# Optimization experiments

Measured on AMD Instinct MI355X. Metric: run time of the kernel, lower is better.

The kernel has to match this reference:

```python
import jax, jax.numpy as jnp
import numpy as np

EMBED_DIMS = 192
NUM_HEADS = 6
WH, WW = 7, 7
N_TOK = WH * WW
B_WIN = 4096


def _rpe_index(Wh, Ww):
    coords = np.array([[x, y] for x in range(Ww) for y in range(Wh)])  # [N,2]
    d = coords[None, :, :] - coords[:, None, :]                        # [N,N,2]
    idx = (d[:, :, 0] + Ww - 1) * (2 * Ww - 1) + (d[:, :, 1] + Wh - 1)
    return idx.T  # transpose(0,1) as in the torch code


def setup_inputs() -> dict:
    key = jax.random.key(0)
    ks = jax.random.split(key, 6)
    C = EMBED_DIMS
    return {
        "x": jax.random.normal(ks[0], (B_WIN, N_TOK, C), dtype=jnp.float32),
        "qkv_w": jax.random.normal(ks[1], (3 * C, C), dtype=jnp.float32) * 0.02,
        "qkv_b": jax.random.normal(ks[2], (3 * C,), dtype=jnp.float32) * 0.02,
        "proj_w": jax.random.normal(ks[3], (C, C), dtype=jnp.float32) * 0.02,
        "proj_b": jax.random.normal(ks[4], (C,), dtype=jnp.float32) * 0.02,
        "rpe_table": jax.random.normal(ks[5], ((2 * WH - 1) * (2 * WW - 1), NUM_HEADS), dtype=jnp.float32),
        "rpe_idx": jnp.asarray(_rpe_index(WH, WW), dtype=jnp.int32),
    }


def reference(x, qkv_w, qkv_b, proj_w, proj_b, rpe_table, rpe_idx):
    B, N, C = x.shape
    H = NUM_HEADS
    hd = C // H
    scale = hd ** -0.5
    # qkv projection: torch Linear is x @ W.T + b
    qkv = x @ qkv_w.T + qkv_b                      # [B, N, 3C]
    qkv = qkv.reshape(B, N, 3, H, hd).transpose(2, 0, 3, 1, 4)  # [3, B, H, N, hd]
    q, k, v = qkv[0] * scale, qkv[1], qkv[2]
    attn = jnp.einsum("bhnd,bhmd->bhnm", q, k)     # [B, H, N, N]
    # relative position bias gather: table[idx] -> [N, N, H] -> [H, N, N]
    bias = rpe_table[rpe_idx].transpose(2, 0, 1)
    attn = jax.nn.softmax(attn + bias, axis=-1)
    out = jnp.einsum("bhnm,bhmd->bhnd", attn, v)   # [B, H, N, hd]
    out = out.transpose(0, 2, 1, 3).reshape(B, N, C)
    return out @ proj_w.T + proj_b
```

## Files before the change

kernel.cpp:

```cpp
#include <hip/hip_runtime.h>
#include <stdint.h>

#define NWIN 4096
#define NTOK 49
#define CDIM 192
#define NH   6
#define HD   32

typedef __attribute__((ext_vector_type(8))) short short8;
typedef __attribute__((ext_vector_type(4))) float floatx4;
typedef unsigned short ushort_t;
typedef unsigned int uint32;

#define XS_S 200
#define QK_S 296
#define P_S  72
#define VT_S 72

__device__ __forceinline__ ushort_t f2bf(float f) {
    uint32 u = __float_as_uint(f);
    u += 0x7fffu + ((u >> 16) & 1u);
    return (ushort_t)(u >> 16);
}

__global__ void wmsa_prologue(const float* __restrict__ qkv_w,
                              const float* __restrict__ proj_w,
                              const float* __restrict__ rpe_table,
                              const int*   __restrict__ rpe_idx,
                              ushort_t* __restrict__ qkv_wb,
                              ushort_t* __restrict__ proj_wb,
                              float* __restrict__ biasws)
{
    int i = blockIdx.x * 256 + threadIdx.x;
    if (i < 110592) {
        qkv_wb[i] = f2bf(qkv_w[i]);
    } else if (i < 147456) {
        proj_wb[i - 110592] = f2bf(proj_w[i - 110592]);
    } else if (i < 147456 + NH * NTOK * 64) {
        int r = i - 147456;
        int h = r / (NTOK * 64);
        int rem = r - h * (NTOK * 64);
        int n = rem >> 6, m = rem & 63;
        biasws[r] = (m < NTOK) ? rpe_table[rpe_idx[n * NTOK + m] * NH + h] : 0.f;
    }
}

__global__ __launch_bounds__(256)
void wmsa_mfma(const float* __restrict__ x,
               const ushort_t* __restrict__ qkv_wb,
               const float* __restrict__ qkv_b,
               const ushort_t* __restrict__ proj_wb,
               const float* __restrict__ proj_b,
               const float* __restrict__ biasws,
               float* __restrict__ out)
{
    __shared__ alignas(16) ushort_t reg0[NTOK * XS_S];
    __shared__ alignas(16) ushort_t qkvs[NTOK * QK_S];
    __shared__ alignas(16) ushort_t Pb[NTOK * P_S];
    __shared__ alignas(16) ushort_t Vt[HD * VT_S];

    const int b    = blockIdx.x;
    const int t    = threadIdx.x;
    const int w    = t >> 6;
    const int lane = t & 63;
    const int quad = lane >> 4;
    const int c    = lane & 15;
    const float scale = 0.17677669529663687f;

    const float* xb = x + (size_t)b * (NTOK * CDIM);

    for (int i = t; i < (NTOK * CDIM) / 4; i += 256) {
        int e = i * 4;
        int n = e / CDIM, d = e - n * CDIM;
        float4 v = *(const float4*)(xb + e);
        ushort_t* p = &reg0[n * XS_S + d];
        p[0] = f2bf(v.x); p[1] = f2bf(v.y); p[2] = f2bf(v.z); p[3] = f2bf(v.w);
    }
    __syncthreads();

    short8 afr[4][6];
    #pragma unroll
    for (int mt = 0; mt < 4; ++mt) {
        int row = mt * 16 + c;
        #pragma unroll
        for (int ks = 0; ks < 6; ++ks)
            afr[mt][ks] = *(const short8*)&reg0[row * XS_S + ks * 32 + quad * 8];
    }

    for (int pass = 0; pass < 2; ++pass) {
        for (int nt = w; nt < 18; nt += 4) {
            int s_idx = nt / 6;
            int rem   = nt - s_idx * 6;
            int hh    = rem >> 1;
            int half  = nt & 1;
            int jrow  = s_idx * CDIM + (3 * pass + hh) * HD + half * 16 + c;
            const ushort_t* bp = qkv_wb + jrow * CDIM + quad * 8;

            floatx4 z = {0.f, 0.f, 0.f, 0.f};
            floatx4 acc[4];
            #pragma unroll
            for (int mt = 0; mt < 4; ++mt) acc[mt] = z;

            #pragma unroll
            for (int ks = 0; ks < 6; ++ks) {
                short8 bf = *(const short8*)(bp + ks * 32);
                #pragma unroll
                for (int mt = 0; mt < 4; ++mt)
                    acc[mt] = __builtin_amdgcn_mfma_f32_16x16x32_bf16(
                        afr[mt][ks], bf, acc[mt], 0, 0, 0);
            }

            float bias = qkv_b[jrow];
            float mul  = (s_idx == 0) ? scale : 1.f;
            int ecol   = s_idx * 96 + hh * HD + half * 16 + c;
            #pragma unroll
            for (int mt = 0; mt < 4; ++mt) {
                #pragma unroll
                for (int r = 0; r < 4; ++r) {
                    int n = mt * 16 + quad * 4 + r;
                    if (n < NTOK)
                        qkvs[n * QK_S + ecol] = f2bf((acc[mt][r] + bias) * mul);
                }
            }
        }
        __syncthreads();

        for (int hh = 0; hh < 3; ++hh) {
            int h = pass * 3 + hh;

            short8 aq = *(const short8*)&qkvs[(w * 16 + c) * QK_S + hh * HD + quad * 8];
            floatx4 sacc[4];
            #pragma unroll
            for (int nt = 0; nt < 4; ++nt) {
                short8 bk = *(const short8*)&qkvs[(nt * 16 + c) * QK_S + 96 + hh * HD + quad * 8];
                floatx4 z = {0.f, 0.f, 0.f, 0.f};
                sacc[nt] = __builtin_amdgcn_mfma_f32_16x16x32_bf16(aq, bk, z, 0, 0, 0);
            }

            const float* bpb = biasws + h * (NTOK * 64);
            #pragma unroll
            for (int r = 0; r < 4; ++r) {
                int n  = w * 16 + quad * 4 + r;
                int nc = (n < NTOK) ? n : (NTOK - 1);
                float sv[4];
                #pragma unroll
                for (int nt = 0; nt < 4; ++nt) {
                    int col = nt * 16 + c;
                    float bias = bpb[nc * 64 + col];
                    sv[nt] = (col < NTOK) ? (sacc[nt][r] + bias) : -1e30f;
                }
                float m0 = fmaxf(fmaxf(sv[0], sv[1]), fmaxf(sv[2], sv[3]));
                m0 = fmaxf(m0, __shfl_xor(m0, 1));
                m0 = fmaxf(m0, __shfl_xor(m0, 2));
                m0 = fmaxf(m0, __shfl_xor(m0, 4));
                m0 = fmaxf(m0, __shfl_xor(m0, 8));
                float ex[4], s0 = 0.f;
                #pragma unroll
                for (int nt = 0; nt < 4; ++nt) { ex[nt] = __expf(sv[nt] - m0); s0 += ex[nt]; }
                s0 += __shfl_xor(s0, 1);
                s0 += __shfl_xor(s0, 2);
                s0 += __shfl_xor(s0, 4);
                s0 += __shfl_xor(s0, 8);
                float inv = 1.f / s0;
                if (n < NTOK) {
                    #pragma unroll
                    for (int nt = 0; nt < 4; ++nt)
                        Pb[n * P_S + nt * 16 + c] = f2bf(ex[nt] * inv);
                }
            }

            for (int i = t; i < HD * 64; i += 256) {
                int d = i >> 6, m = i & 63;
                Vt[d * VT_S + m] = (m < NTOK)
                    ? qkvs[m * QK_S + 192 + hh * HD + d] : (ushort_t)0;
            }
            __syncthreads();

            floatx4 z2 = {0.f, 0.f, 0.f, 0.f};
            floatx4 oacc[2]; oacc[0] = z2; oacc[1] = z2;
            #pragma unroll
            for (int ks = 0; ks < 2; ++ks) {
                short8 ap = *(const short8*)&Pb[(w * 16 + c) * P_S + ks * 32 + quad * 8];
                #pragma unroll
                for (int nt = 0; nt < 2; ++nt) {
                    short8 bv = *(const short8*)&Vt[(nt * 16 + c) * VT_S + ks * 32 + quad * 8];
                    oacc[nt] = __builtin_amdgcn_mfma_f32_16x16x32_bf16(ap, bv, oacc[nt], 0, 0, 0);
                }
            }
            #pragma unroll
            for (int nt = 0; nt < 2; ++nt) {
                #pragma unroll
                for (int r = 0; r < 4; ++r) {
                    int n = w * 16 + quad * 4 + r;
                    if (n < NTOK)
                        reg0[n * XS_S + h * HD + nt * 16 + c] = f2bf(oacc[nt][r]);
                }
            }
            __syncthreads();
        }
    }

    short8 aof[4][6];
    #pragma unroll
    for (int mt = 0; mt < 4; ++mt) {
        int row = mt * 16 + c;
        #pragma unroll
        for (int ks = 0; ks < 6; ++ks)
            aof[mt][ks] = *(const short8*)&reg0[row * XS_S + ks * 32 + quad * 8];
    }
    for (int nt = w; nt < 12; nt += 4) {
        int j = nt * 16 + c;
        const ushort_t* bp = proj_wb + j * CDIM + quad * 8;
        floatx4 z = {0.f, 0.f, 0.f, 0.f};
        floatx4 acc[4];
        #pragma unroll
        for (int mt = 0; mt < 4; ++mt) acc[mt] = z;
        #pragma unroll
        for (int ks = 0; ks < 6; ++ks) {
            short8 bf = *(const short8*)(bp + ks * 32);
            #pragma unroll
            for (int mt = 0; mt < 4; ++mt)
                acc[mt] = __builtin_amdgcn_mfma_f32_16x16x32_bf16(
                    aof[mt][ks], bf, acc[mt], 0, 0, 0);
        }
        float pb = proj_b[j];
        #pragma unroll
        for (int mt = 0; mt < 4; ++mt) {
            #pragma unroll
            for (int r = 0; r < 4; ++r) {
                int n = mt * 16 + quad * 4 + r;
                if (n < NTOK)
                    out[((size_t)b * NTOK + n) * CDIM + j] = acc[mt][r] + pb;
            }
        }
    }
}

extern "C" void kernel_launch(void* const* d_in, const int* in_sizes, int n_in,
                              void* d_out, int out_size, void* d_ws, size_t ws_size,
                              hipStream_t stream)
{
    const float* x      = (const float*)d_in[0];
    const float* qkv_w  = (const float*)d_in[1];
    const float* qkv_b  = (const float*)d_in[2];
    const float* proj_w = (const float*)d_in[3];
    const float* proj_b = (const float*)d_in[4];
    const float* rpe_t  = (const float*)d_in[5];
    const int*   rpe_i  = (const int*)d_in[6];
    float*       o      = (float*)d_out;

    ushort_t* qkv_wb  = (ushort_t*)d_ws;
    ushort_t* proj_wb = qkv_wb + 110592;
    float*    biasws  = (float*)((char*)d_ws + (110592 + 36864) * sizeof(ushort_t));

    int tot = 147456 + NH * NTOK * 64;
    wmsa_prologue<<<dim3((tot + 255) / 256), dim3(256), 0, stream>>>(
        qkv_w, proj_w, rpe_t, rpe_i, qkv_wb, proj_wb, biasws);
    wmsa_mfma<<<dim3(NWIN), dim3(256), 0, stream>>>(
        x, qkv_wb, qkv_b, proj_wb, proj_b, biasws, o);
}
```

Measured before the change: 593.9 us.

## Write V transposed in the QKV epilogue, regroup heads, and shrink shared memory

The QKV projection now runs in three passes of two heads each instead of two passes of three. The V part of its output goes straight into a transposed shared-memory buffer from the GEMM epilogue, and Q and K are interleaved per head in a smaller buffer. This removes the per-head V transpose loop and two block-wide barriers per head, keeping one barrier per pass. Shared memory is packed into a single smaller array, which may let more blocks fit on each compute unit. The cost is one extra pass of weight-fragment loads and a single sync point per pass.

```diff
diff --git a/kernel.cpp b/kernel.cpp
--- a/kernel.cpp
+++ b/kernel.cpp
@@ -13,9 +13,15 @@
 typedef unsigned int uint32;
 
 #define XS_S 200
-#define QK_S 296
+#define QK_S 136
 #define P_S  72
 #define VT_S 72
+
+#define OFF_REG0 0
+#define OFF_QKS  9800
+#define OFF_PB   16464
+#define OFF_VT   19992
+#define LDS_TOT  24600
 
 __device__ __forceinline__ ushort_t f2bf(float f) {
     uint32 u = __float_as_uint(f);
@@ -54,10 +60,11 @@
                const float* __restrict__ biasws,
                float* __restrict__ out)
 {
-    __shared__ alignas(16) ushort_t reg0[NTOK * XS_S];
-    __shared__ alignas(16) ushort_t qkvs[NTOK * QK_S];
-    __shared__ alignas(16) ushort_t Pb[NTOK * P_S];
-    __shared__ alignas(16) ushort_t Vt[HD * VT_S];
+    __shared__ alignas(16) ushort_t lds[LDS_TOT];
+    ushort_t* const reg0 = lds + OFF_REG0;
+    ushort_t* const qks  = lds + OFF_QKS;
+    ushort_t* const Pb   = lds + OFF_PB;
+    ushort_t* const Vt   = lds + OFF_VT;
 
     const int b    = blockIdx.x;
     const int t    = threadIdx.x;
@@ -87,13 +94,13 @@
             afr[mt][ks] = *(const short8*)&reg0[row * XS_S + ks * 32 + quad * 8];
     }
 
-    for (int pass = 0; pass < 2; ++pass) {
-        for (int nt = w; nt < 18; nt += 4) {
-            int s_idx = nt / 6;
-            int rem   = nt - s_idx * 6;
+    for (int pass = 0; pass < 3; ++pass) {
+        for (int nt = w; nt < 12; nt += 4) {
+            int s_idx = nt >> 2;
+            int rem   = nt & 3;
             int hh    = rem >> 1;
-            int half  = nt & 1;
-            int jrow  = s_idx * CDIM + (3 * pass + hh) * HD + half * 16 + c;
+            int half  = rem & 1;
+            int jrow  = s_idx * CDIM + (2 * pass + hh) * HD + half * 16 + c;
             const ushort_t* bp = qkv_wb + jrow * CDIM + quad * 8;
 
             floatx4 z = {0.f, 0.f, 0.f, 0.f};
@@ -111,28 +118,41 @@
             }
 
             float bias = qkv_b[jrow];
-            float mul  = (s_idx == 0) ? scale : 1.f;
-            int ecol   = s_idx * 96 + hh * HD + half * 16 + c;
-            #pragma unroll
-            for (int mt = 0; mt < 4; ++mt) {
-                #pragma unroll
-                for (int r = 0; r < 4; ++r) {
-                    int n = mt * 16 + quad * 4 + r;
-                    if (n < NTOK)
-                        qkvs[n * QK_S + ecol] = f2bf((acc[mt][r] + bias) * mul);
+            if (s_idx == 2) {
+                int vrow = hh * HD + half * 16 + c;
+                #pragma unroll
+                for (int mt = 0; mt < 4; ++mt) {
+                    #pragma unroll
+                    for (int r = 0; r < 4; ++r) {
+                        int n = mt * 16 + quad * 4 + r;
+                        Vt[vrow * VT_S + n] =
+                            (n < NTOK) ? f2bf(acc[mt][r] + bias) : (ushort_t)0;
+                    }
+                }
+            } else {
+                float mul = (s_idx == 0) ? scale : 1.f;
+                int ecol  = hh * 64 + s_idx * 32 + half * 16 + c;
+                #pragma unroll
+                for (int mt = 0; mt < 4; ++mt) {
+                    #pragma unroll
+                    for (int r = 0; r < 4; ++r) {
+                        int n = mt * 16 + quad * 4 + r;
+                        if (n < NTOK)
+                            qks[n * QK_S + ecol] = f2bf((acc[mt][r] + bias) * mul);
+                    }
                 }
             }
         }
         __syncthreads();
 
-        for (int hh = 0; hh < 3; ++hh) {
-            int h = pass * 3 + hh;
-
-            short8 aq = *(const short8*)&qkvs[(w * 16 + c) * QK_S + hh * HD + quad * 8];
+        for (int hh = 0; hh < 2; ++hh) {
+            int h = pass * 2 + hh;
+
+            short8 aq = *(const short8*)&qks[(w * 16 + c) * QK_S + hh * 64 + quad * 8];
             floatx4 sacc[4];
             #pragma unroll
             for (int nt = 0; nt < 4; ++nt) {
-                short8 bk = *(const short8*)&qkvs[(nt * 16 + c) * QK_S + 96 + hh * HD + quad * 8];
+                short8 bk = *(const short8*)&qks[(nt * 16 + c) * QK_S + hh * 64 + 32 + quad * 8];
                 floatx4 z = {0.f, 0.f, 0.f, 0.f};
                 sacc[nt] = __builtin_amdgcn_mfma_f32_16x16x32_bf16(aq, bk, z, 0, 0, 0);
             }
@@ -169,13 +189,6 @@
                 }
             }
 
-            for (int i = t; i < HD * 64; i += 256) {
-                int d = i >> 6, m = i & 63;
-                Vt[d * VT_S + m] = (m < NTOK)
-                    ? qkvs[m * QK_S + 192 + hh * HD + d] : (ushort_t)0;
-            }
-            __syncthreads();
-
             floatx4 z2 = {0.f, 0.f, 0.f, 0.f};
             floatx4 oacc[2]; oacc[0] = z2; oacc[1] = z2;
             #pragma unroll
@@ -183,7 +196,7 @@
                 short8 ap = *(const short8*)&Pb[(w * 16 + c) * P_S + ks * 32 + quad * 8];
                 #pragma unroll
                 for (int nt = 0; nt < 2; ++nt) {
-                    short8 bv = *(const short8*)&Vt[(nt * 16 + c) * VT_S + ks * 32 + quad * 8];
+                    short8 bv = *(const short8*)&Vt[(hh * HD + nt * 16 + c) * VT_S + ks * 32 + quad * 8];
                     oacc[nt] = __builtin_amdgcn_mfma_f32_16x16x32_bf16(ap, bv, oacc[nt], 0, 0, 0);
                 }
             }
@@ -196,8 +209,8 @@
                         reg0[n * XS_S + h * HD + nt * 16 + c] = f2bf(oacc[nt][r]);
                 }
             }
-            __syncthreads();
-        }
+        }
+        __syncthreads();
     }
 
     short8 aof[4][6];
```

Result: faster. 555.0 us (-6.5%).
